# Kernel optimization log

Hardware: AMD Instinct MI355X
Metric: run time of the kernel (lower is better)

Reference implementation:

```python
import jax, jax.numpy as jnp
import numpy as np

N, H, W, D, K = 32, 36, 36, 512, 64
POOL = 3  # pool_list=[3] -> 3x3 grid of regions
EPS = 1e-12


def setup_inputs() -> dict:
    key = jax.random.key(0)
    k1, k2, k3 = jax.random.split(key, 3)
    x = jax.random.normal(k1, (N, H, W, D), dtype=jnp.float32)
    W_conv = jax.random.normal(k2, (D, K), dtype=jnp.float32) * 0.05
    C = jax.random.normal(k3, (D, K), dtype=jnp.float32) * 0.05
    return {"x": x, "W_conv": W_conv, "C": C}


def _l2norm(v, axis):
    return v / jnp.sqrt(jnp.sum(v * v, axis=axis, keepdims=True) + EPS)


def _encode_vlad(xm, W_conv, C):
    # xm: [N, h, w, D]
    s = jnp.einsum('nhwd,dk->nhwk', xm, W_conv)          # 1x1 conv, no bias
    a = jax.nn.softmax(s, axis=-1)                        # soft assignment [N,h,w,K]
    # Faithful to sum_hw a * (x[...,None] - C) without the [N,h,w,D,K] blow-up:
    # = einsum(x, a) - C * sum_hw(a)
    asum = jnp.sum(a, axis=(1, 2))                        # [N, K]
    v = jnp.einsum('nhwd,nhwk->ndk', xm, a) - C[None] * asum[:, None, :]  # [N, D, K]
    # intra-normalization: normalize each cluster's residual over D
    v = _l2norm(v, axis=1)                                # [N, D, K]
    v = v.reshape(v.shape[0], -1)                         # flatten (row-major, matches tf)
    v = _l2norm(v, axis=-1)                               # [N, D*K]
    return v


def reference(x, W_conv, C):
    n, h, w, d = x.shape
    rl, cl = h / POOL, w / POOL
    outs = []
    for jy in range(POOL):
        for ix in range(POOL):
            y1, y2 = int(round(jy * rl)), int(round(jy * rl + rl))
            x1, x2 = int(round(ix * cl)), int(round(ix * cl + cl))
            outs.append(_encode_vlad(x[:, y1:y2, x1:x2, :], W_conv, C))
    return jnp.concatenate(outs, axis=1)  # [N, POOL*POOL*D*K]
```

## Files before the change

kernel.cpp:

```cpp
#include <hip/hip_runtime.h>

typedef __attribute__((ext_vector_type(4))) float f32x4;
typedef __attribute__((ext_vector_type(8))) short short8;

#define EPSF 1e-12f

__device__ __forceinline__ ushort bf16rne(float x) {
  uint u = __float_as_uint(x);
  u += 0x7fffu + ((u >> 16) & 1u);
  return (ushort)(u >> 16);
}
__device__ __forceinline__ float bf2f(ushort h) {
  return __uint_as_float(((uint)h) << 16);
}
__device__ __forceinline__ f32x4 mfma16(short8 a, short8 b, f32x4 c) {
  return __builtin_amdgcn_mfma_f32_16x16x32_bf16(a, b, c, 0, 0, 0);
}
__device__ __forceinline__ short8 frag64(const ushort* base, int row, int kofs) {
  int g = kofs >> 3;
  int sg = g ^ (row & 7);
  return *(const short8*)(base + row * 64 + (sg << 3));
}

__global__ __launch_bounds__(256) void k0_wt(const float* __restrict__ W,
                                             ushort* __restrict__ wsWT) {
  int k = blockIdx.x;
  for (int d = threadIdx.x; d < 512; d += 256) {
    float v = W[(size_t)d * 64 + k];
    ushort h = bf16rne(v);
    wsWT[k * 512 + d] = h;
    wsWT[32768 + k * 512 + d] = bf16rne(v - bf2f(h));
  }
}

__global__ __launch_bounds__(512) void k1_assign(const float* __restrict__ x,
                                                 const ushort* __restrict__ wsWT,
                                                 float4* __restrict__ aT_ws,
                                                 float* __restrict__ asum_ws) {
  __shared__ char sm[53504];
  ushort* xsH = (ushort*)(sm);
  ushort* xsL = (ushort*)(sm + 18432);
  ushort* wtH = (ushort*)(sm + 36864);
  ushort* wtL = (ushort*)(sm + 45056);
  ushort* atH = (ushort*)(sm);
  ushort* atL = (ushort*)(sm + 18432);
  float* asumS = (float*)(sm + 53248);

  int b = blockIdx.x;
  int n = b / 9, r = b % 9;
  int y1 = (r / 3) * 12, x1 = (r % 3) * 12;
  int t = threadIdx.x;
  int w = t >> 6;
  int lane = t & 63, l15 = lane & 15, hi16 = lane >> 4;
  const float* xn = x + (size_t)n * (36 * 36 * 512);
  if (t < 64) asumS[t] = 0.f;

  float4 px[3][2];
  short8 pwH, pwL;
  int ntask = (t < 128) ? 3 : 2;
  int wk = t >> 3, wg = t & 7;

  f32x4 acc[4][2];
#pragma unroll
  for (int mi = 0; mi < 4; ++mi) {
    acc[mi][0] = (f32x4){0.f, 0.f, 0.f, 0.f};
    acc[mi][1] = (f32x4){0.f, 0.f, 0.f, 0.f};
  }

  {
    int d0 = 0;
#pragma unroll
    for (int i = 0; i < 3; ++i)
      if (i < ntask) {
        int task = t + i * 512;
        int p = task >> 3, g = task & 7;
        const float* src = xn + ((size_t)(y1 + p / 12) * 36 + (x1 + p % 12)) * 512 + d0 + g * 8;
        px[i][0] = *(const float4*)src;
        px[i][1] = *(const float4*)(src + 4);
      }
    pwH = *(const short8*)(wsWT + wk * 512 + d0 + wg * 8);
    pwL = *(const short8*)(wsWT + 32768 + wk * 512 + d0 + wg * 8);
  }

  for (int c = 0; c < 8; ++c) {
    __syncthreads();
#pragma unroll
    for (int i = 0; i < 3; ++i)
      if (i < ntask) {
        int task = t + i * 512;
        int p = task >> 3, g = task & 7;
        float vals[8] = {px[i][0].x, px[i][0].y, px[i][0].z, px[i][0].w,
                         px[i][1].x, px[i][1].y, px[i][1].z, px[i][1].w};
        short8 h8, l8;
#pragma unroll
        for (int j = 0; j < 8; ++j) {
          ushort h = bf16rne(vals[j]);
          h8[j] = (short)h;
          l8[j] = (short)bf16rne(vals[j] - bf2f(h));
        }
        int sg = g ^ (p & 7);
        *(short8*)(xsH + p * 64 + (sg << 3)) = h8;
        *(short8*)(xsL + p * 64 + (sg << 3)) = l8;
      }
    {
      int sg = wg ^ (wk & 7);
      *(short8*)(wtH + wk * 64 + (sg << 3)) = pwH;
      *(short8*)(wtL + wk * 64 + (sg << 3)) = pwL;
    }
    if (c < 7) {
      int d0 = (c + 1) * 64;
#pragma unroll
      for (int i = 0; i < 3; ++i)
        if (i < ntask) {
          int task = t + i * 512;
          int p = task >> 3, g = task & 7;
          const float* src = xn + ((size_t)(y1 + p / 12) * 36 + (x1 + p % 12)) * 512 + d0 + g * 8;
          px[i][0] = *(const float4*)src;
          px[i][1] = *(const float4*)(src + 4);
        }
      pwH = *(const short8*)(wsWT + wk * 512 + d0 + wg * 8);
      pwL = *(const short8*)(wsWT + 32768 + wk * 512 + d0 + wg * 8);
    }
    __syncthreads();

#pragma unroll
    for (int ks = 0; ks < 2; ++ks) {
      int kofs = ks * 32 + hi16 * 8;
      short8 aH[4], aL[4];
#pragma unroll
      for (int mi = 0; mi < 4; ++mi) {
        aH[mi] = frag64(wtH, mi * 16 + l15, kofs);
        aL[mi] = frag64(wtL, mi * 16 + l15, kofs);
      }
      {
        short8 bH = frag64(xsH, w * 16 + l15, kofs);
        short8 bL = frag64(xsL, w * 16 + l15, kofs);
#pragma unroll
        for (int mi = 0; mi < 4; ++mi) {
          f32x4 a0 = acc[mi][0];
          a0 = mfma16(aH[mi], bH, a0);
          a0 = mfma16(aH[mi], bL, a0);
          a0 = mfma16(aL[mi], bH, a0);
          acc[mi][0] = a0;
        }
      }
      if (w == 0) {
        short8 bH = frag64(xsH, 128 + l15, kofs);
        short8 bL = frag64(xsL, 128 + l15, kofs);
#pragma unroll
        for (int mi = 0; mi < 4; ++mi) {
          f32x4 a0 = acc[mi][1];
          a0 = mfma16(aH[mi], bH, a0);
          a0 = mfma16(aH[mi], bL, a0);
          a0 = mfma16(aL[mi], bH, a0);
          acc[mi][1] = a0;
        }
      }
    }
  }
  __syncthreads();

  float part[4][4];
#pragma unroll
  for (int mi = 0; mi < 4; ++mi)
#pragma unroll
    for (int rr = 0; rr < 4; ++rr) part[mi][rr] = 0.f;

  {
    int p = w * 16 + l15;
    float m = -1e30f;
#pragma unroll
    for (int mi = 0; mi < 4; ++mi)
#pragma unroll
      for (int rr = 0; rr < 4; ++rr) m = fmaxf(m, acc[mi][0][rr]);
    m = fmaxf(m, __shfl_xor(m, 16));
    m = fmaxf(m, __shfl_xor(m, 32));
    float e[4][4], sum = 0.f;
#pragma unroll
    for (int mi = 0; mi < 4; ++mi)
#pragma unroll
      for (int rr = 0; rr < 4; ++rr) {
        e[mi][rr] = __expf(acc[mi][0][rr] - m);
        sum += e[mi][rr];
      }
    sum += __shfl_xor(sum, 16);
    sum += __shfl_xor(sum, 32);
    float inv = 1.f / sum;
    int gp = p >> 3, pl = p & 7;
#pragma unroll
    for (int mi = 0; mi < 4; ++mi)
#pragma unroll
      for (int rr = 0; rr < 4; ++rr) {
        float a = e[mi][rr] * inv;
        part[mi][rr] += a;
        int k = mi * 16 + hi16 * 4 + rr;
        int sg = gp ^ (k & 7);
        int idx = k * 144 + (sg << 3) + pl;
        ushort h = bf16rne(a);
        atH[idx] = h;
        atL[idx] = bf16rne(a - bf2f(h));
      }
  }
  if (w == 0) {
    int p = 128 + l15;
    float m = -1e30f;
#pragma unroll
    for (int mi = 0; mi < 4; ++mi)
#pragma unroll
      for (int rr = 0; rr < 4; ++rr) m = fmaxf(m, acc[mi][1][rr]);
    m = fmaxf(m, __shfl_xor(m, 16));
    m = fmaxf(m, __shfl_xor(m, 32));
    float e[4][4], sum = 0.f;
#pragma unroll
    for (int mi = 0; mi < 4; ++mi)
#pragma unroll
      for (int rr = 0; rr < 4; ++rr) {
        e[mi][rr] = __expf(acc[mi][1][rr] - m);
        sum += e[mi][rr];
      }
    sum += __shfl_xor(sum, 16);
    sum += __shfl_xor(sum, 32);
    float inv = 1.f / sum;
    int gp = p >> 3, pl = p & 7;
#pragma unroll
    for (int mi = 0; mi < 4; ++mi)
#pragma unroll
      for (int rr = 0; rr < 4; ++rr) {
        float a = e[mi][rr] * inv;
        part[mi][rr] += a;
        int k = mi * 16 + hi16 * 4 + rr;
        int idx = k * 144 + (gp << 3) + pl;
        ushort h = bf16rne(a);
        atH[idx] = h;
        atL[idx] = bf16rne(a - bf2f(h));
      }
  }

#pragma unroll
  for (int mi = 0; mi < 4; ++mi)
#pragma unroll
    for (int rr = 0; rr < 4; ++rr) {
      float s = part[mi][rr];
      s += __shfl_xor(s, 1);
      s += __shfl_xor(s, 2);
      s += __shfl_xor(s, 4);
      s += __shfl_xor(s, 8);
      if (l15 == 0) atomicAdd(&asumS[mi * 16 + hi16 * 4 + rr], s);
    }
  __syncthreads();

  {
    float4* dst = aT_ws + (size_t)b * 2432;
    for (int i = t; i < 2432; i += 512) {
      int plane = i / 1216;
      int rem = i - plane * 1216;
      int row = rem / 19, c4 = rem - row * 19;
      float4 v = {0.f, 0.f, 0.f, 0.f};
      if (c4 < 18) {
        int sg = (c4 < 16) ? (c4 ^ (row & 7)) : c4;
        v = *(const float4*)(sm + plane * 18432 + row * 288 + sg * 16);
      }
      dst[i] = v;
    }
    if (t < 64) asum_ws[b * 64 + t] = asumS[t];
  }
}

__global__ __launch_bounds__(512) void k2_vlad(
    const float* __restrict__ x, const float* __restrict__ C,
    const float4* __restrict__ aT_ws, const float* __restrict__ asum_ws,
    float* __restrict__ out, float* __restrict__ colnorm) {
  __shared__ float4 smv[2504];
  char* sm = (char*)smv;
  ushort* atH = (ushort*)sm;
  ushort* atL = (ushort*)(sm + 19456);
  int* poff = (int*)(sm + 38912);
  float* asumS = (float*)(sm + 39552);
  float* cn2 = (float*)(sm + 39808);

  int b = blockIdx.x;
  int reg = b % 288;
  int dc = b / 288;
  int n = reg / 9, r = reg % 9;
  int d0 = dc * 64;
  int y1 = (r / 3) * 12, x1 = (r % 3) * 12;
  int t = threadIdx.x;
  int w = t >> 6, lane = t & 63, l15 = lane & 15, hi16 = lane >> 4;
  const float* xn = x + (size_t)n * (36 * 36 * 512);

  if (t < 160) poff[t] = (t < 144) ? ((y1 + t / 12) * 36 + (x1 + t % 12)) * 512 : 0;
  if (t < 64) {
    asumS[t] = asum_ws[reg * 64 + t];
    cn2[t] = 0.f;
  }
  {
    const float4* src = aT_ws + (size_t)reg * 2432;
    for (int i = t; i < 2432; i += 512) smv[i] = src[i];
  }
  __syncthreads();

  int mi = w & 3, kh = w >> 2;
  int drow = d0 + mi * 16 + l15;
  const float* xcol = xn + drow;

  f32x4 acc[2];
  acc[0] = (f32x4){0.f, 0.f, 0.f, 0.f};
  acc[1] = (f32x4){0.f, 0.f, 0.f, 0.f};

#pragma unroll
  for (int ks = 0; ks < 5; ++ks) {
    int pb = ks * 32 + hi16 * 8;
    int4 poA = *reinterpret_cast<const int4*>(&poff[pb]);
    int4 poB = *reinterpret_cast<const int4*>(&poff[pb + 4]);
    float av[8];
    av[0] = xcol[poA.x]; av[1] = xcol[poA.y];
    av[2] = xcol[poA.z]; av[3] = xcol[poA.w];
    av[4] = xcol[poB.x]; av[5] = xcol[poB.y];
    av[6] = xcol[poB.z]; av[7] = xcol[poB.w];
    bool valid = (ks < 4) || (hi16 < 2);
    short8 ah, al;
#pragma unroll
    for (int j = 0; j < 8; ++j) {
      float v = valid ? av[j] : 0.f;
      ushort h = bf16rne(v);
      ah[j] = (short)h;
      al[j] = (short)bf16rne(v - bf2f(h));
    }
#pragma unroll
    for (int ni = 0; ni < 2; ++ni) {
      int row = kh * 32 + ni * 16 + l15;
      short8 bh = *(const short8*)(atH + row * 152 + pb);
      short8 bl = *(const short8*)(atL + row * 152 + pb);
      f32x4 a0 = acc[ni];
      a0 = mfma16(ah, bh, a0);
      a0 = mfma16(ah, bl, a0);
      a0 = mfma16(al, bh, a0);
      acc[ni] = a0;
    }
  }

  size_t obase = (size_t)reg * (512 * 64);
#pragma unroll
  for (int ni = 0; ni < 2; ++ni) {
    int k = kh * 32 + ni * 16 + l15;
    float ak = asumS[k];
    float s2 = 0.f;
#pragma unroll
    for (int rr = 0; rr < 4; ++rr) {
      int d = d0 + mi * 16 + hi16 * 4 + rr;
      float v = acc[ni][rr] - C[(size_t)d * 64 + k] * ak;
      out[obase + (size_t)d * 64 + k] = v;
      s2 += v * v;
    }
    atomicAdd(&cn2[k], s2);
  }
  __syncthreads();
  if (t < 64) atomicAdd(&colnorm[reg * 64 + t], cn2[t]);
}

__global__ __launch_bounds__(256) void k3_scale(float* __restrict__ out,
                                                const float* __restrict__ colnorm) {
  int b = blockIdx.x;
  int reg = b % 288;
  int dc = b / 288;

  __shared__ float ratio[64];
  __shared__ float fs[64];
  int t = threadIdx.x;
  float c = 0.f;
  if (t < 64) {
    c = colnorm[reg * 64 + t];
    ratio[t] = c / (c + EPSF);
  }
  __syncthreads();
  if (t < 64) {
    float g = 0.f;
#pragma unroll
    for (int j = 0; j < 64; ++j) g += ratio[j];
    fs[t] = rsqrtf(c + EPSF) * rsqrtf(g + EPSF);
  }
  __syncthreads();

  size_t base4 = (((size_t)reg * 512) + (size_t)dc * 128) * 64 / 4;
  float4* o4 = reinterpret_cast<float4*>(out);
  for (int j = 0; j < 8; ++j) {
    size_t idx = base4 + t + 256 * j;
    float4 v = o4[idx];
    int k0 = (int)((idx * 4) & 63);
    v.x *= fs[k0]; v.y *= fs[k0 + 1]; v.z *= fs[k0 + 2]; v.w *= fs[k0 + 3];
    o4[idx] = v;
  }
}

extern "C" void kernel_launch(void* const* d_in, const int* in_sizes, int n_in,
                              void* d_out, int out_size, void* d_ws, size_t ws_size,
                              hipStream_t stream) {
  const float* x = (const float*)d_in[0];
  const float* Wc = (const float*)d_in[1];
  const float* C = (const float*)d_in[2];
  float* out = (float*)d_out;

  char* ws = (char*)d_ws;
  ushort* wsWT = (ushort*)(ws);
  float* asum_ws = (float*)(ws + 131072);
  float* colnorm = (float*)(ws + 204800);
  float4* aT_ws = (float4*)(ws + 278528);

  hipMemsetAsync(colnorm, 0, 288 * 64 * sizeof(float), stream);
  k0_wt<<<64, 256, 0, stream>>>(Wc, wsWT);
  k1_assign<<<288, 512, 0, stream>>>(x, wsWT, aT_ws, asum_ws);
  k2_vlad<<<2304, 512, 0, stream>>>(x, C, aT_ws, asum_ws, out, colnorm);
  k3_scale<<<1152, 256, 0, stream>>>(out, colnorm);
}
```

Before: 86.32 us.

## Split assignment kernel per half-region and drop atomics/memset for column norms

k1_assign now launches two 256-thread blocks per region, each handling 72 pixels, with the wave-to-cluster mapping transposed. The softmax now reduces across waves through shared-memory max and sum buffers. This doubles the block count to fill more CUs and shrinks shared memory per block, at the cost of extra cross-wave syncs. Partial asums and per-chunk column norms are written to separate slots and summed by the consumers, which removes the memset and the global atomics. k2 also gets an occupancy hint in its launch bounds.

```diff
diff --git a/kernel.cpp b/kernel.cpp
--- a/kernel.cpp
+++ b/kernel.cpp
@@ -33,53 +33,55 @@
   }
 }
 
-__global__ __launch_bounds__(512) void k1_assign(const float* __restrict__ x,
-                                                 const ushort* __restrict__ wsWT,
-                                                 float4* __restrict__ aT_ws,
-                                                 float* __restrict__ asum_ws) {
-  __shared__ char sm[53504];
+__global__ __launch_bounds__(256, 4) void k1_assign(
+    const float* __restrict__ x, const ushort* __restrict__ wsWT,
+    float4* __restrict__ aT_ws, float* __restrict__ asum_ws) {
+  __shared__ char sm[37376];
   ushort* xsH = (ushort*)(sm);
-  ushort* xsL = (ushort*)(sm + 18432);
-  ushort* wtH = (ushort*)(sm + 36864);
-  ushort* wtL = (ushort*)(sm + 45056);
+  ushort* xsL = (ushort*)(sm + 9216);
+  ushort* wtH = (ushort*)(sm + 18432);
+  ushort* wtL = (ushort*)(sm + 26624);
+  float* smax = (float*)(sm + 34816);
+  float* ssum = (float*)(sm + 36096);
   ushort* atH = (ushort*)(sm);
-  ushort* atL = (ushort*)(sm + 18432);
-  float* asumS = (float*)(sm + 53248);
+  ushort* atL = (ushort*)(sm + 9216);
 
   int b = blockIdx.x;
-  int n = b / 9, r = b % 9;
+  int region = b >> 1, phalf = b & 1;
+  int n = region / 9, r = region % 9;
   int y1 = (r / 3) * 12, x1 = (r % 3) * 12;
+  int p0 = phalf * 72;
   int t = threadIdx.x;
   int w = t >> 6;
   int lane = t & 63, l15 = lane & 15, hi16 = lane >> 4;
   const float* xn = x + (size_t)n * (36 * 36 * 512);
-  if (t < 64) asumS[t] = 0.f;
 
   float4 px[3][2];
-  short8 pwH, pwL;
-  int ntask = (t < 128) ? 3 : 2;
-  int wk = t >> 3, wg = t & 7;
-
-  f32x4 acc[4][2];
-#pragma unroll
-  for (int mi = 0; mi < 4; ++mi) {
-    acc[mi][0] = (f32x4){0.f, 0.f, 0.f, 0.f};
-    acc[mi][1] = (f32x4){0.f, 0.f, 0.f, 0.f};
-  }
+  short8 pwH[2], pwL[2];
+  int ntask = (t < 64) ? 3 : 2;
+
+  f32x4 acc[5];
+#pragma unroll
+  for (int ni = 0; ni < 5; ++ni) acc[ni] = (f32x4){0.f, 0.f, 0.f, 0.f};
 
   {
-    int d0 = 0;
 #pragma unroll
     for (int i = 0; i < 3; ++i)
       if (i < ntask) {
-        int task = t + i * 512;
+        int task = t + i * 256;
         int p = task >> 3, g = task & 7;
-        const float* src = xn + ((size_t)(y1 + p / 12) * 36 + (x1 + p % 12)) * 512 + d0 + g * 8;
+        int pr = p0 + p;
+        const float* src = xn + ((size_t)(y1 + pr / 12) * 36 + (x1 + pr % 12)) * 512 + g * 8;
         px[i][0] = *(const float4*)src;
         px[i][1] = *(const float4*)(src + 4);
       }
-    pwH = *(const short8*)(wsWT + wk * 512 + d0 + wg * 8);
-    pwL = *(const short8*)(wsWT + 32768 + wk * 512 + d0 + wg * 8);
+#pragma unroll
+    for (int i = 0; i < 2; ++i) {
+      int task = t + i * 256;
+      int wk = task >> 3, wg = task & 7;
+      pwH[i] = *(const short8*)(wsWT + wk * 512 + wg * 8);
+      pwL[i] = *(const short8*)(wsWT + 32768 + wk * 512 + wg * 8);
+    }
   }
 
   for (int c = 0; c < 8; ++c) {
@@ -87,7 +89,7 @@
 #pragma unroll
     for (int i = 0; i < 3; ++i)
       if (i < ntask) {
-        int task = t + i * 512;
+        int task = t + i * 256;
         int p = task >> 3, g = task & 7;
         float vals[8] = {px[i][0].x, px[i][0].y, px[i][0].z, px[i][0].w,
                          px[i][1].x, px[i][1].y, px[i][1].z, px[i][1].w};
@@ -102,171 +104,141 @@
         *(short8*)(xsH + p * 64 + (sg << 3)) = h8;
         *(short8*)(xsL + p * 64 + (sg << 3)) = l8;
       }
-    {
+#pragma unroll
+    for (int i = 0; i < 2; ++i) {
+      int task = t + i * 256;
+      int wk = task >> 3, wg = task & 7;
       int sg = wg ^ (wk & 7);
-      *(short8*)(wtH + wk * 64 + (sg << 3)) = pwH;
-      *(short8*)(wtL + wk * 64 + (sg << 3)) = pwL;
+      *(short8*)(wtH + wk * 64 + (sg << 3)) = pwH[i];
+      *(short8*)(wtL + wk * 64 + (sg << 3)) = pwL[i];
     }
     if (c < 7) {
       int d0 = (c + 1) * 64;
 #pragma unroll
       for (int i = 0; i < 3; ++i)
         if (i < ntask) {
-          int task = t + i * 512;
+          int task = t + i * 256;
           int p = task >> 3, g = task & 7;
-          const float* src = xn + ((size_t)(y1 + p / 12) * 36 + (x1 + p % 12)) * 512 + d0 + g * 8;
+          int pr = p0 + p;
+          const float* src = xn + ((size_t)(y1 + pr / 12) * 36 + (x1 + pr % 12)) * 512 + d0 + g * 8;
           px[i][0] = *(const float4*)src;
           px[i][1] = *(const float4*)(src + 4);
         }
-      pwH = *(const short8*)(wsWT + wk * 512 + d0 + wg * 8);
-      pwL = *(const short8*)(wsWT + 32768 + wk * 512 + d0 + wg * 8);
+#pragma unroll
+      for (int i = 0; i < 2; ++i) {
+        int task = t + i * 256;
+        int wk = task >> 3, wg = task & 7;
+        pwH[i] = *(const short8*)(wsWT + wk * 512 + d0 + wg * 8);
+        pwL[i] = *(const short8*)(wsWT + 32768 + wk * 512 + d0 + wg * 8);
+      }
     }
     __syncthreads();
 
 #pragma unroll
     for (int ks = 0; ks < 2; ++ks) {
       int kofs = ks * 32 + hi16 * 8;
-      short8 aH[4], aL[4];
-#pragma unroll
-      for (int mi = 0; mi < 4; ++mi) {
-        aH[mi] = frag64(wtH, mi * 16 + l15, kofs);
-        aL[mi] = frag64(wtL, mi * 16 + l15, kofs);
-      }
-      {
-        short8 bH = frag64(xsH, w * 16 + l15, kofs);
-        short8 bL = frag64(xsL, w * 16 + l15, kofs);
-#pragma unroll
-        for (int mi = 0; mi < 4; ++mi) {
-          f32x4 a0 = acc[mi][0];
-          a0 = mfma16(aH[mi], bH, a0);
-          a0 = mfma16(aH[mi], bL, a0);
-          a0 = mfma16(aL[mi], bH, a0);
-          acc[mi][0] = a0;
-        }
-      }
-      if (w == 0) {
-        short8 bH = frag64(xsH, 128 + l15, kofs);
-        short8 bL = frag64(xsL, 128 + l15, kofs);
-#pragma unroll
-        for (int mi = 0; mi < 4; ++mi) {
-          f32x4 a0 = acc[mi][1];
-          a0 = mfma16(aH[mi], bH, a0);
-          a0 = mfma16(aH[mi], bL, a0);
-          a0 = mfma16(aL[mi], bH, a0);
-          acc[mi][1] = a0;
-        }
-      }
-    }
-  }
-  __syncthreads();
-
-  float part[4][4];
-#pragma unroll
-  for (int mi = 0; mi < 4; ++mi)
-#pragma unroll
-    for (int rr = 0; rr < 4; ++rr) part[mi][rr] = 0.f;
-
-  {
-    int p = w * 16 + l15;
-    float m = -1e30f;
-#pragma unroll
-    for (int mi = 0; mi < 4; ++mi)
-#pragma unroll
-      for (int rr = 0; rr < 4; ++rr) m = fmaxf(m, acc[mi][0][rr]);
+      short8 aH = frag64(wtH, w * 16 + l15, kofs);
+      short8 aL = frag64(wtL, w * 16 + l15, kofs);
+#pragma unroll
+      for (int ni = 0; ni < 5; ++ni) {
+        short8 bH = frag64(xsH, ni * 16 + l15, kofs);
+        short8 bL = frag64(xsL, ni * 16 + l15, kofs);
+        f32x4 a0 = acc[ni];
+        a0 = mfma16(aH, bH, a0);
+        a0 = mfma16(aH, bL, a0);
+        a0 = mfma16(aL, bH, a0);
+        acc[ni] = a0;
+      }
+    }
+  }
+  __syncthreads();
+
+  float lm[5];
+#pragma unroll
+  for (int ni = 0; ni < 5; ++ni) {
+    float m = fmaxf(fmaxf(acc[ni][0], acc[ni][1]), fmaxf(acc[ni][2], acc[ni][3]));
     m = fmaxf(m, __shfl_xor(m, 16));
     m = fmaxf(m, __shfl_xor(m, 32));
-    float e[4][4], sum = 0.f;
-#pragma unroll
-    for (int mi = 0; mi < 4; ++mi)
+    lm[ni] = m;
+  }
+  if (hi16 == 0)
+#pragma unroll
+    for (int ni = 0; ni < 5; ++ni) smax[w * 80 + ni * 16 + l15] = lm[ni];
+  __syncthreads();
+
+  float e[5][4], ls[5];
+#pragma unroll
+  for (int ni = 0; ni < 5; ++ni) {
+    int p = ni * 16 + l15;
+    float M = fmaxf(fmaxf(smax[0 * 80 + p], smax[1 * 80 + p]),
+                    fmaxf(smax[2 * 80 + p], smax[3 * 80 + p]));
+    float s = 0.f;
+#pragma unroll
+    for (int rr = 0; rr < 4; ++rr) {
+      e[ni][rr] = __expf(acc[ni][rr] - M);
+      s += e[ni][rr];
+    }
+    s += __shfl_xor(s, 16);
+    s += __shfl_xor(s, 32);
+    ls[ni] = s;
+  }
+  if (hi16 == 0)
+#pragma unroll
+    for (int ni = 0; ni < 5; ++ni) ssum[w * 80 + ni * 16 + l15] = ls[ni];
+  __syncthreads();
+
+  float part[4];
+#pragma unroll
+  for (int rr = 0; rr < 4; ++rr) part[rr] = 0.f;
+
+#pragma unroll
+  for (int ni = 0; ni < 5; ++ni) {
+    int p = ni * 16 + l15;
+    if (p < 72) {
+      float S = ssum[0 * 80 + p] + ssum[1 * 80 + p] + ssum[2 * 80 + p] + ssum[3 * 80 + p];
+      float inv = 1.f / S;
 #pragma unroll
       for (int rr = 0; rr < 4; ++rr) {
-        e[mi][rr] = __expf(acc[mi][0][rr] - m);
-        sum += e[mi][rr];
-      }
-    sum += __shfl_xor(sum, 16);
-    sum += __shfl_xor(sum, 32);
-    float inv = 1.f / sum;
-    int gp = p >> 3, pl = p & 7;
-#pragma unroll
-    for (int mi = 0; mi < 4; ++mi)
-#pragma unroll
-      for (int rr = 0; rr < 4; ++rr) {
-        float a = e[mi][rr] * inv;
-        part[mi][rr] += a;
-        int k = mi * 16 + hi16 * 4 + rr;
-        int sg = gp ^ (k & 7);
-        int idx = k * 144 + (sg << 3) + pl;
+        float a = e[ni][rr] * inv;
+        part[rr] += a;
+        int k = w * 16 + hi16 * 4 + rr;
         ushort h = bf16rne(a);
-        atH[idx] = h;
-        atL[idx] = bf16rne(a - bf2f(h));
-      }
-  }
-  if (w == 0) {
-    int p = 128 + l15;
-    float m = -1e30f;
-#pragma unroll
-    for (int mi = 0; mi < 4; ++mi)
-#pragma unroll
-      for (int rr = 0; rr < 4; ++rr) m = fmaxf(m, acc[mi][1][rr]);
-    m = fmaxf(m, __shfl_xor(m, 16));
-    m = fmaxf(m, __shfl_xor(m, 32));
-    float e[4][4], sum = 0.f;
-#pragma unroll
-    for (int mi = 0; mi < 4; ++mi)
-#pragma unroll
-      for (int rr = 0; rr < 4; ++rr) {
-        e[mi][rr] = __expf(acc[mi][1][rr] - m);
-        sum += e[mi][rr];
-      }
-    sum += __shfl_xor(sum, 16);
-    sum += __shfl_xor(sum, 32);
-    float inv = 1.f / sum;
-    int gp = p >> 3, pl = p & 7;
-#pragma unroll
-    for (int mi = 0; mi < 4; ++mi)
-#pragma unroll
-      for (int rr = 0; rr < 4; ++rr) {
-        float a = e[mi][rr] * inv;
-        part[mi][rr] += a;
-        int k = mi * 16 + hi16 * 4 + rr;
-        int idx = k * 144 + (gp << 3) + pl;
-        ushort h = bf16rne(a);
-        atH[idx] = h;
-        atL[idx] = bf16rne(a - bf2f(h));
-      }
-  }
-
-#pragma unroll
-  for (int mi = 0; mi < 4; ++mi)
-#pragma unroll
-    for (int rr = 0; rr < 4; ++rr) {
-      float s = part[mi][rr];
-      s += __shfl_xor(s, 1);
-      s += __shfl_xor(s, 2);
-      s += __shfl_xor(s, 4);
-      s += __shfl_xor(s, 8);
-      if (l15 == 0) atomicAdd(&asumS[mi * 16 + hi16 * 4 + rr], s);
-    }
+        atH[k * 72 + p] = h;
+        atL[k * 72 + p] = bf16rne(a - bf2f(h));
+      }
+    }
+  }
+#pragma unroll
+  for (int rr = 0; rr < 4; ++rr) {
+    float s = part[rr];
+    s += __shfl_xor(s, 1);
+    s += __shfl_xor(s, 2);
+    s += __shfl_xor(s, 4);
+    s += __shfl_xor(s, 8);
+    if (l15 == 0) asum_ws[b * 64 + w * 16 + hi16 * 4 + rr] = s;
+  }
   __syncthreads();
 
   {
-    float4* dst = aT_ws + (size_t)b * 2432;
-    for (int i = t; i < 2432; i += 512) {
-      int plane = i / 1216;
-      int rem = i - plane * 1216;
-      int row = rem / 19, c4 = rem - row * 19;
-      float4 v = {0.f, 0.f, 0.f, 0.f};
-      if (c4 < 18) {
-        int sg = (c4 < 16) ? (c4 ^ (row & 7)) : c4;
-        v = *(const float4*)(sm + plane * 18432 + row * 288 + sg * 16);
-      }
-      dst[i] = v;
-    }
-    if (t < 64) asum_ws[b * 64 + t] = asumS[t];
-  }
-}
-
-__global__ __launch_bounds__(512) void k2_vlad(
+    float4* dst = aT_ws + (size_t)region * 2432;
+    for (int i = t; i < 1152; i += 256) {
+      int plane = i / 576;
+      int rem = i - plane * 576;
+      int row = rem / 9, c4 = rem - row * 9;
+      float4 v = *(const float4*)(sm + plane * 9216 + row * 144 + c4 * 16);
+      dst[plane * 1216 + row * 19 + phalf * 9 + c4] = v;
+    }
+    if (phalf) {
+      float4 z = {0.f, 0.f, 0.f, 0.f};
+      for (int i = t; i < 128; i += 256) {
+        int plane = i >> 6, row = i & 63;
+        dst[plane * 1216 + row * 19 + 18] = z;
+      }
+    }
+  }
+}
+
+__global__ __launch_bounds__(512, 8) void k2_vlad(
     const float* __restrict__ x, const float* __restrict__ C,
     const float4* __restrict__ aT_ws, const float* __restrict__ asum_ws,
     float* __restrict__ out, float* __restrict__ colnorm) {
@@ -290,7 +262,7 @@
 
   if (t < 160) poff[t] = (t < 144) ? ((y1 + t / 12) * 36 + (x1 + t % 12)) * 512 : 0;
   if (t < 64) {
-    asumS[t] = asum_ws[reg * 64 + t];
+    asumS[t] = asum_ws[(reg * 2) * 64 + t] + asum_ws[(reg * 2 + 1) * 64 + t];
     cn2[t] = 0.f;
   }
   {
@@ -355,7 +327,7 @@
     atomicAdd(&cn2[k], s2);
   }
   __syncthreads();
-  if (t < 64) atomicAdd(&colnorm[reg * 64 + t], cn2[t]);
+  if (t < 64) colnorm[(size_t)(reg * 8 + dc) * 64 + t] = cn2[t];
 }
 
 __global__ __launch_bounds__(256) void k3_scale(float* __restrict__ out,
@@ -369,7 +341,8 @@
   int t = threadIdx.x;
   float c = 0.f;
   if (t < 64) {
-    c = colnorm[reg * 64 + t];
+#pragma unroll
+    for (int j = 0; j < 8; ++j) c += colnorm[(size_t)(reg * 8 + j) * 64 + t];
     ratio[t] = c / (c + EPSF);
   }
   __syncthreads();
@@ -403,12 +376,11 @@
   char* ws = (char*)d_ws;
   ushort* wsWT = (ushort*)(ws);
   float* asum_ws = (float*)(ws + 131072);
-  float* colnorm = (float*)(ws + 204800);
-  float4* aT_ws = (float4*)(ws + 278528);
-
-  hipMemsetAsync(colnorm, 0, 288 * 64 * sizeof(float), stream);
+  float* colnorm = (float*)(ws + 278528);
+  float4* aT_ws = (float4*)(ws + 868352);
+
   k0_wt<<<64, 256, 0, stream>>>(Wc, wsWT);
-  k1_assign<<<288, 512, 0, stream>>>(x, wsWT, aT_ws, asum_ws);
+  k1_assign<<<576, 256, 0, stream>>>(x, wsWT, aT_ws, asum_ws);
   k2_vlad<<<2304, 512, 0, stream>>>(x, C, aT_ws, asum_ws, out, colnorm);
   k3_scale<<<1152, 256, 0, stream>>>(out, colnorm);
 }
```

Result: faster. 80.07 us (-7.2%).
